# Performance work log

Hardware: AMD Instinct MI355X
Metric: run time of the kernel (lower is better)

Reference implementation:

```python
import jax, jax.numpy as jnp
import numpy as np
import math

B, T, C = 2, 2048, 1024
H = 16
D = C // H


def setup_inputs() -> dict:
    key = jax.random.key(0)
    ks = jax.random.split(key, 5)
    s = 1.0 / math.sqrt(C)
    return {
        "x": jax.random.normal(ks[0], (B, T, C), dtype=jnp.float32),
        "W_qkv": jax.random.normal(ks[1], (C, 3 * C), dtype=jnp.float32) * s,
        "b_qkv": jnp.zeros((3 * C,), dtype=jnp.float32),
        "W_proj": jax.random.normal(ks[2], (C, C), dtype=jnp.float32) * s,
        "b_proj": jnp.zeros((C,), dtype=jnp.float32),
    }


def reference(x, W_qkv, b_qkv, W_proj, b_proj):
    qkv = x @ W_qkv + b_qkv  # [B,T,3C]
    q, k, v = jnp.split(qkv, 3, axis=-1)
    # [B,T,C] -> [B,H,T,D]
    q = q.reshape(B, T, H, D).transpose(0, 2, 1, 3)
    k = k.reshape(B, T, H, D).transpose(0, 2, 1, 3)
    v = v.reshape(B, T, H, D).transpose(0, 2, 1, 3)
    sm_scale = 1.0 / math.sqrt(D)
    att = jnp.einsum("bhqd,bhkd->bhqk", q, k) * sm_scale
    causal = jnp.tril(jnp.ones((T, T), dtype=bool))  # True = keep
    att = jnp.where(causal, att, -jnp.inf)
    att = jax.nn.softmax(att, axis=-1)
    y = jnp.einsum("bhqk,bhkd->bhqd", att, v)  # [B,H,T,D]
    y = y.transpose(0, 2, 1, 3).reshape(B, T, C)
    return y @ W_proj + b_proj
```

## Files before the change

kernel.cpp:

```cpp
#include <hip/hip_runtime.h>
#include <hip/hip_bf16.h>
#include <math.h>

#define BB 2
#define TT 2048
#define CCH 1024
#define HH 16
#define DD 64
#define BT (BB*TT)
#define N3 (3*CCH)

typedef __attribute__((ext_vector_type(8))) short short8;
typedef __attribute__((ext_vector_type(4))) float f32x4;
typedef __attribute__((ext_vector_type(16))) float f32x16;

__device__ __forceinline__ unsigned short f2bf(float f) {
  unsigned int u = __float_as_uint(f);
  unsigned int r = (u + 0x7FFFu + ((u >> 16) & 1u)) >> 16;
  return (unsigned short)r;
}
__device__ __forceinline__ int cvtpk(float lo, float hi) {
  int r;
  asm("v_cvt_pk_bf16_f32 %0, %1, %2" : "=v"(r) : "v"(lo), "v"(hi));
  return r;
}
__device__ __forceinline__ void plswap(int &a, int &b) {
  asm("v_permlane32_swap_b32 %0, %1" : "+v"(a), "+v"(b));
}
__device__ __forceinline__ float fexp2(float x) {
  float r;
  asm("v_exp_f32 %0, %1" : "=v"(r) : "v"(x));
  return r;
}
__device__ __forceinline__ void gload_lds16(const unsigned short* g, unsigned short* l) {
  __builtin_amdgcn_global_load_lds((const __attribute__((address_space(1))) void*)g,
                                   (__attribute__((address_space(3))) void*)l, 16, 0, 0);
}
__device__ __forceinline__ float fmax3(float a, float b, float c) {
  return fmaxf(fmaxf(a, b), c);
}


__global__ __launch_bounds__(256) void k_prep(const float* __restrict__ x,
                                              const float* __restrict__ W_qkv,
                                              const float* __restrict__ W_proj,
                                              unsigned short* __restrict__ Xb,
                                              unsigned short* __restrict__ Wt_qkv,
                                              unsigned short* __restrict__ Wt_proj) {
  __shared__ float tile[32][33];
  int id = blockIdx.x;
  int tid = threadIdx.x;
  if (id < 2048) {
    int i = id * 256 + tid;
    const float4 a = *(const float4*)(x + (size_t)i * 8);
    const float4 b = *(const float4*)(x + (size_t)i * 8 + 4);
    short8 v;
    v[0] = f2bf(a.x); v[1] = f2bf(a.y); v[2] = f2bf(a.z); v[3] = f2bf(a.w);
    v[4] = f2bf(b.x); v[5] = f2bf(b.y); v[6] = f2bf(b.z); v[7] = f2bf(b.w);
    *(short8*)(Xb + (size_t)i * 8) = v;
    return;
  }
  const float* in;
  unsigned short* out;
  int R, Cn, tc, tr;
  if (id < 2048 + 3072) {
    int u = id - 2048;
    in = W_qkv; out = Wt_qkv; R = CCH; Cn = N3;
    tc = (u % 96) * 32; tr = (u / 96) * 32;
  } else {
    int u = id - 5120;
    in = W_proj; out = Wt_proj; R = CCH; Cn = CCH;
    tc = (u % 32) * 32; tr = (u / 32) * 32;
  }
  int lx = tid & 31;
  int ly = tid >> 5;
#pragma unroll
  for (int i = 0; i < 32; i += 8)
    tile[ly + i][lx] = in[(size_t)(tr + ly + i) * Cn + tc + lx];
  __syncthreads();
#pragma unroll
  for (int i = 0; i < 32; i += 8)
    out[(size_t)(tc + ly + i) * R + tr + lx] = f2bf(tile[lx][ly + i]);
}

__global__ __launch_bounds__(256) void k_qkv_gemm(const unsigned short* __restrict__ Xb,
                                                  const unsigned short* __restrict__ Wt,
                                                  const float* __restrict__ bias,
                                                  unsigned short* __restrict__ Qf,
                                                  unsigned short* __restrict__ Kf,
                                                  unsigned short* __restrict__ Vf) {
  __shared__ __align__(16) unsigned short As[128 * 32];
  __shared__ __align__(16) unsigned short Bs[128 * 32];
  int tid = threadIdx.x;
  int mb = blockIdx.x * 128;
  int nb = blockIdx.y * 128;
  int wid = tid >> 6, lane = tid & 63;
  int wr = (wid >> 1) * 64, wc = (wid & 1) * 64;
  int l15 = lane & 15, l4 = lane >> 4;
  int l16 = lane >> 2, lc = (lane & 3) * 8;
  f32x4 acc[4][4];
#pragma unroll
  for (int a = 0; a < 4; ++a)
#pragma unroll
    for (int b = 0; b < 4; ++b)
#pragma unroll
      for (int j = 0; j < 4; ++j) acc[a][b][j] = 0.0f;

  for (int kb = 0; kb < CCH; kb += 32) {
#pragma unroll
    for (int i = 0; i < 2; ++i) {
      int arow = wid * 32 + i * 16;
      gload_lds16(Xb + (size_t)(mb + arow + l16) * CCH + kb + lc, &As[arow * 32]);
      gload_lds16(Wt + (size_t)(nb + arow + l16) * CCH + kb + lc, &Bs[arow * 32]);
    }
    __syncthreads();
    short8 af[4], bfr[4];
#pragma unroll
    for (int mt = 0; mt < 4; ++mt) af[mt] = *(const short8*)(&As[(wr + mt * 16 + l15) * 32 + l4 * 8]);
#pragma unroll
    for (int nt = 0; nt < 4; ++nt) bfr[nt] = *(const short8*)(&Bs[(wc + nt * 16 + l15) * 32 + l4 * 8]);
#pragma unroll
    for (int mt = 0; mt < 4; ++mt)
#pragma unroll
      for (int nt = 0; nt < 4; ++nt)
        acc[mt][nt] = __builtin_amdgcn_mfma_f32_16x16x32_bf16(af[mt], bfr[nt], acc[mt][nt], 0, 0, 0);
    __syncthreads();
  }

#pragma unroll
  for (int mt = 0; mt < 4; ++mt) {
#pragma unroll
    for (int nt = 0; nt < 4; ++nt) {
      int gcol = nb + wc + nt * 16 + l15;
      int which = gcol >> 10;
      int cc = gcol & 1023;
      int hh = cc >> 6, d = cc & 63;
      float bv = bias[gcol];
#pragma unroll
      for (int j = 0; j < 4; ++j) {
        int grow = mb + wr + mt * 16 + l4 * 4 + j;
        int b = grow >> 11, t = grow & 2047;
        float v = acc[mt][nt][j] + bv;
        size_t bh = (size_t)(b * HH + hh) * TT * DD;
        if (which == 2) {
          size_t a = (size_t)((((t >> 6) * 2 + (d >> 5)) * 4 + ((t >> 4) & 3)) * 512
                             + (((t >> 3) & 1) * 32 + (d & 31)) * 8 + (t & 7));
          Vf[bh + a] = f2bf(v);
        } else {
          size_t a = (size_t)(((t >> 5) * 4 + (d >> 4)) * 512
                             + ((d >> 3) & 1) * 256 + (t & 31) * 8 + (d & 7));
          if (which == 0) Qf[bh + a] = f2bf(v * 0.18033688f);
          else            Kf[bh + a] = f2bf(v);
        }
      }
    }
  }
}

__global__ __launch_bounds__(128) void k_attn(const unsigned short* __restrict__ Qf,
                                              const unsigned short* __restrict__ Kf,
                                              const unsigned short* __restrict__ Vf,
                                              unsigned short* __restrict__ Y) {
  __shared__ float ex[64 * 33];
  __shared__ float exml[128];
  int tid = threadIdx.x;
  int jx = blockIdx.x;
  int j = 63 - (jx >> 5);
  int bh = jx & 31;
  int wid = tid >> 6, lane = tid & 63;
  int l31 = lane & 31, h = lane >> 5;
  int q0 = j * 32;
  int qrow = q0 + l31;
  int tmax = j >> 1;

  const unsigned short* Qp = Qf + (size_t)bh * TT * DD;
  const unsigned short* Kp = Kf + (size_t)bh * TT * DD;
  const unsigned short* Vp = Vf + (size_t)bh * TT * DD;

  short8 qf[4];
#pragma unroll
  for (int m = 0; m < 4; ++m)
    qf[m] = *(const short8*)(Qp + (size_t)(j * 4 + m) * 512 + lane * 8);

  f32x16 zv;
#pragma unroll
  for (int r = 0; r < 16; ++r) zv[r] = 0.0f;
  f32x16 po[2];
  po[0] = zv; po[1] = zv;
  float mrun = -1e30f, lrun = 0.0f;

  for (int t = wid; t <= tmax; t += 2) {
    int kvb = t * 64;

    short8 kf[2][4];
#pragma unroll
    for (int t32 = 0; t32 < 2; ++t32)
#pragma unroll
      for (int m = 0; m < 4; ++m)
        kf[t32][m] = *(const short8*)(Kp + (size_t)((t * 2 + t32) * 4 + m) * 512 + lane * 8);

    f32x16 st[2];
    __builtin_amdgcn_s_setprio(1);
#pragma unroll
    for (int t32 = 0; t32 < 2; ++t32) {
      st[t32] = __builtin_amdgcn_mfma_f32_32x32x16_bf16(kf[t32][0], qf[0], zv, 0, 0, 0);
#pragma unroll
      for (int m = 1; m < 4; ++m)
        st[t32] = __builtin_amdgcn_mfma_f32_32x32x16_bf16(kf[t32][m], qf[m], st[t32], 0, 0, 0);
    }
    __builtin_amdgcn_s_setprio(0);

    short8 vf[2][4];
#pragma unroll
    for (int dt = 0; dt < 2; ++dt)
#pragma unroll
      for (int g = 0; g < 4; ++g)
        vf[dt][g] = *(const short8*)(Vp + (size_t)((t * 2 + dt) * 4 + g) * 512 + lane * 8);

    if (kvb + 63 > q0) {
#pragma unroll
      for (int t32 = 0; t32 < 2; ++t32)
#pragma unroll
        for (int r = 0; r < 16; ++r) {
          int kvg = kvb + t32 * 32 + (r & 3) + 8 * (r >> 2) + 4 * h;
          if (kvg > qrow) st[t32][r] = -1e30f;
        }
    }

    float A = st[0][0], B = st[0][1], C = st[0][2], Dv = st[0][3];
#pragma unroll
    for (int r = 4; r < 16; r += 4) {
      A = fmax3(A, st[0][r], st[0][r + 1]);
      B = fmax3(B, st[0][r + 2], st[0][r + 3]);
      C = fmax3(C, st[1][r - 4], st[1][r - 3]);
      Dv = fmax3(Dv, st[1][r - 2], st[1][r - 1]);
    }
    C = fmax3(C, st[1][12], st[1][13]);
    Dv = fmax3(Dv, st[1][14], st[1][15]);
    float mx = fmaxf(fmax3(A, B, C), Dv);
    mx = fmaxf(mx, __shfl_xor(mx, 32));

    if (__any(mx - mrun > 8.0f)) {
      float mnew = fmaxf(mrun, mx);
      float alpha = fexp2(mrun - mnew);
      lrun *= alpha;
#pragma unroll
      for (int dt = 0; dt < 2; ++dt)
#pragma unroll
        for (int r = 0; r < 16; ++r) po[dt][r] *= alpha;
      mrun = mnew;
    }

    float sum = 0.0f;
#pragma unroll
    for (int t32 = 0; t32 < 2; ++t32)
#pragma unroll
      for (int r = 0; r < 16; ++r) {
        float p = fexp2(st[t32][r] - mrun);
        st[t32][r] = p;
        sum += p;
      }
    sum += __shfl_xor(sum, 32);
    lrun += sum;

    short8 pf[4];
#pragma unroll
    for (int g = 0; g < 4; ++g) {
      int t32 = g >> 1, r0 = (g & 1) * 8;
      int a = cvtpk(st[t32][r0 + 0], st[t32][r0 + 1]);
      int b = cvtpk(st[t32][r0 + 4], st[t32][r0 + 5]);
      plswap(a, b);
      int c = cvtpk(st[t32][r0 + 2], st[t32][r0 + 3]);
      int d = cvtpk(st[t32][r0 + 6], st[t32][r0 + 7]);
      plswap(c, d);
      union { int w[4]; short8 s; } un;
      un.w[0] = a; un.w[1] = c; un.w[2] = b; un.w[3] = d;
      pf[g] = un.s;
    }

    __builtin_amdgcn_s_setprio(1);
#pragma unroll
    for (int dt = 0; dt < 2; ++dt)
#pragma unroll
      for (int g = 0; g < 4; ++g)
        po[dt] = __builtin_amdgcn_mfma_f32_32x32x16_bf16(vf[dt][g], pf[g], po[dt], 0, 0, 0);
    __builtin_amdgcn_s_setprio(0);
  }

  __syncthreads();
  if (wid == 1) {
#pragma unroll
    for (int dt = 0; dt < 2; ++dt)
#pragma unroll
      for (int r = 0; r < 16; ++r) ex[lane * 33 + dt * 16 + r] = po[dt][r];
    exml[lane] = mrun;
    exml[64 + lane] = lrun;
  }
  __syncthreads();
  if (wid == 0) {
    float m1 = exml[lane], l1 = exml[64 + lane];
    float M = fmaxf(mrun, m1);
    float a0 = fexp2(mrun - M), a1 = fexp2(m1 - M);
    float inv = 1.0f / (lrun * a0 + l1 * a1);
    a0 *= inv; a1 *= inv;
    int b = bh >> 4, hh = bh & 15;
    unsigned short* yp = Y + ((size_t)(b * TT + qrow)) * CCH + hh * DD;
#pragma unroll
    for (int dt = 0; dt < 2; ++dt)
#pragma unroll
      for (int r = 0; r < 16; r += 2) {
        int d = dt * 32 + (r & 3) + 8 * (r >> 2) + 4 * h;
        float v0 = po[dt][r]     * a0 + ex[lane * 33 + dt * 16 + r]     * a1;
        float v1 = po[dt][r + 1] * a0 + ex[lane * 33 + dt * 16 + r + 1] * a1;
        *(int*)(yp + d) = cvtpk(v0, v1);
      }
  }
}

__global__ __launch_bounds__(256) void k_proj_gemm(const unsigned short* __restrict__ Yb,
                                                   const unsigned short* __restrict__ Wt,
                                                   const float* __restrict__ bias,
                                                   float* __restrict__ Out) {
  __shared__ __align__(16) unsigned short As[128 * 32];
  __shared__ __align__(16) unsigned short Bs[128 * 32];
  int tid = threadIdx.x;
  int mb = blockIdx.x * 128;
  int nb = blockIdx.y * 128;
  int wid = tid >> 6, lane = tid & 63;
  int wr = (wid >> 1) * 64, wc = (wid & 1) * 64;
  int l15 = lane & 15, l4 = lane >> 4;
  int l16 = lane >> 2, lc = (lane & 3) * 8;
  f32x4 acc[4][4];
#pragma unroll
  for (int a = 0; a < 4; ++a)
#pragma unroll
    for (int b = 0; b < 4; ++b)
#pragma unroll
      for (int j = 0; j < 4; ++j) acc[a][b][j] = 0.0f;

  for (int kb = 0; kb < CCH; kb += 32) {
#pragma unroll
    for (int i = 0; i < 2; ++i) {
      int arow = wid * 32 + i * 16;
      gload_lds16(Yb + (size_t)(mb + arow + l16) * CCH + kb + lc, &As[arow * 32]);
      gload_lds16(Wt + (size_t)(nb + arow + l16) * CCH + kb + lc, &Bs[arow * 32]);
    }
    __syncthreads();
    short8 af[4], bfr[4];
#pragma unroll
    for (int mt = 0; mt < 4; ++mt) af[mt] = *(const short8*)(&As[(wr + mt * 16 + l15) * 32 + l4 * 8]);
#pragma unroll
    for (int nt = 0; nt < 4; ++nt) bfr[nt] = *(const short8*)(&Bs[(wc + nt * 16 + l15) * 32 + l4 * 8]);
#pragma unroll
    for (int mt = 0; mt < 4; ++mt)
#pragma unroll
      for (int nt = 0; nt < 4; ++nt)
        acc[mt][nt] = __builtin_amdgcn_mfma_f32_16x16x32_bf16(af[mt], bfr[nt], acc[mt][nt], 0, 0, 0);
    __syncthreads();
  }

#pragma unroll
  for (int mt = 0; mt < 4; ++mt) {
#pragma unroll
    for (int nt = 0; nt < 4; ++nt) {
      int gcol = nb + wc + nt * 16 + l15;
      float bv = bias[gcol];
#pragma unroll
      for (int j = 0; j < 4; ++j) {
        int grow = mb + wr + mt * 16 + l4 * 4 + j;
        Out[(size_t)grow * CCH + gcol] = acc[mt][nt][j] + bv;
      }
    }
  }
}

extern "C" void kernel_launch(void* const* d_in, const int* in_sizes, int n_in,
                              void* d_out, int out_size, void* d_ws, size_t ws_size,
                              hipStream_t stream) {
  const float* x      = (const float*)d_in[0];
  const float* W_qkv  = (const float*)d_in[1];
  const float* b_qkv  = (const float*)d_in[2];
  const float* W_proj = (const float*)d_in[3];
  const float* b_proj = (const float*)d_in[4];
  float* out = (float*)d_out;

  char* ws = (char*)d_ws;
  size_t off = 0;
  unsigned short* Wt_qkv  = (unsigned short*)(ws + off); off += (size_t)N3 * CCH * 2;
  unsigned short* Wt_proj = (unsigned short*)(ws + off); off += (size_t)CCH * CCH * 2;
  unsigned short* Xb      = (unsigned short*)(ws + off); off += (size_t)BT * CCH * 2;
  unsigned short* Qfb     = (unsigned short*)(ws + off); off += (size_t)BT * CCH * 2;
  unsigned short* Kfb     = (unsigned short*)(ws + off); off += (size_t)BT * CCH * 2;
  unsigned short* Vfb     = (unsigned short*)(ws + off); off += (size_t)BT * CCH * 2;
  unsigned short* Yb      = (unsigned short*)(ws + off); off += (size_t)BT * CCH * 2;

  k_prep<<<dim3(2048 + 3072 + 1024), 256, 0, stream>>>(x, W_qkv, W_proj, Xb, Wt_qkv, Wt_proj);
  k_qkv_gemm<<<dim3(BT / 128, N3 / 128), 256, 0, stream>>>(Xb, Wt_qkv, b_qkv, Qfb, Kfb, Vfb);
  k_attn<<<dim3(2048), 128, 0, stream>>>(Qfb, Kfb, Vfb, Yb);
  k_proj_gemm<<<dim3(BT / 128, CCH / 128), 256, 0, stream>>>(Yb, Wt_proj, b_proj, out);
}
```

Baseline: 104.9 us.

## Double-buffer K/V register loads in attention loop to prefetch next tile

The attention inner loop now issues global loads of the next K/V tile into a second register buffer before computing on the current tile, alternating between two buffers, with sched_barrier to stop the compiler reordering. This hides global load latency behind the MFMA and softmax work of the current tile. In exchange it roughly doubles the registers held for K/V fragments, which could cause spills or lower occupancy.

```diff
diff --git a/kernel.cpp b/kernel.cpp
--- a/kernel.cpp
+++ b/kernel.cpp
@@ -157,6 +157,99 @@
   }
 }
 
+#define AT_ISSUE(KF, VF, tt)                                                                     \
+  {                                                                                              \
+    int _t = (tt);                                                                               \
+    _Pragma("unroll")                                                                            \
+    for (int t32 = 0; t32 < 2; ++t32)                                                            \
+      _Pragma("unroll")                                                                          \
+      for (int m = 0; m < 4; ++m)                                                                \
+        KF[t32][m] = *(const short8*)(Kp + (size_t)((_t * 2 + t32) * 4 + m) * 512 + lane * 8);   \
+    _Pragma("unroll")                                                                            \
+    for (int dt = 0; dt < 2; ++dt)                                                               \
+      _Pragma("unroll")                                                                          \
+      for (int g = 0; g < 4; ++g)                                                                \
+        VF[dt][g] = *(const short8*)(Vp + (size_t)((_t * 2 + dt) * 4 + g) * 512 + lane * 8);     \
+  }
+
+#define AT_COMPUTE(KF, VF, tt)                                                                   \
+  {                                                                                              \
+    int kvb = (tt) * 64;                                                                         \
+    f32x16 st[2];                                                                                \
+    __builtin_amdgcn_s_setprio(1);                                                               \
+    _Pragma("unroll")                                                                            \
+    for (int t32 = 0; t32 < 2; ++t32) {                                                          \
+      st[t32] = __builtin_amdgcn_mfma_f32_32x32x16_bf16(KF[t32][0], qf[0], zv, 0, 0, 0);         \
+      _Pragma("unroll")                                                                          \
+      for (int m = 1; m < 4; ++m)                                                                \
+        st[t32] = __builtin_amdgcn_mfma_f32_32x32x16_bf16(KF[t32][m], qf[m], st[t32], 0, 0, 0);  \
+    }                                                                                            \
+    __builtin_amdgcn_s_setprio(0);                                                               \
+    if (kvb + 63 > q0) {                                                                         \
+      _Pragma("unroll")                                                                          \
+      for (int t32 = 0; t32 < 2; ++t32)                                                          \
+        _Pragma("unroll")                                                                        \
+        for (int r = 0; r < 16; ++r) {                                                           \
+          int kvg = kvb + t32 * 32 + (r & 3) + 8 * (r >> 2) + 4 * h;                             \
+          if (kvg > qrow) st[t32][r] = -1e30f;                                                   \
+        }                                                                                        \
+    }                                                                                            \
+    float A = st[0][0], B = st[0][1], C = st[0][2], Dv = st[0][3];                               \
+    _Pragma("unroll")                                                                            \
+    for (int r = 4; r < 16; r += 4) {                                                            \
+      A = fmax3(A, st[0][r], st[0][r + 1]);                                                      \
+      B = fmax3(B, st[0][r + 2], st[0][r + 3]);                                                  \
+      C = fmax3(C, st[1][r - 4], st[1][r - 3]);                                                  \
+      Dv = fmax3(Dv, st[1][r - 2], st[1][r - 1]);                                                \
+    }                                                                                            \
+    C = fmax3(C, st[1][12], st[1][13]);                                                          \
+    Dv = fmax3(Dv, st[1][14], st[1][15]);                                                        \
+    float mx = fmaxf(fmax3(A, B, C), Dv);                                                        \
+    mx = fmaxf(mx, __shfl_xor(mx, 32));                                                          \
+    if (__any(mx - mrun > 8.0f)) {                                                               \
+      float mnew = fmaxf(mrun, mx);                                                              \
+      float alpha = fexp2(mrun - mnew);                                                          \
+      lrun *= alpha;                                                                             \
+      _Pragma("unroll")                                                                          \
+      for (int dt = 0; dt < 2; ++dt)                                                             \
+        _Pragma("unroll")                                                                        \
+        for (int r = 0; r < 16; ++r) po[dt][r] *= alpha;                                         \
+      mrun = mnew;                                                                               \
+    }                                                                                            \
+    float sum = 0.0f;                                                                            \
+    _Pragma("unroll")                                                                            \
+    for (int t32 = 0; t32 < 2; ++t32)                                                            \
+      _Pragma("unroll")                                                                          \
+      for (int r = 0; r < 16; ++r) {                                                             \
+        float p = fexp2(st[t32][r] - mrun);                                                      \
+        st[t32][r] = p;                                                                          \
+        sum += p;                                                                                \
+      }                                                                                          \
+    sum += __shfl_xor(sum, 32);                                                                  \
+    lrun += sum;                                                                                 \
+    short8 pf[4];                                                                                \
+    _Pragma("unroll")                                                                            \
+    for (int g = 0; g < 4; ++g) {                                                                \
+      int t32 = g >> 1, r0 = (g & 1) * 8;                                                        \
+      int a = cvtpk(st[t32][r0 + 0], st[t32][r0 + 1]);                                           \
+      int b = cvtpk(st[t32][r0 + 4], st[t32][r0 + 5]);                                           \
+      plswap(a, b);                                                                              \
+      int c = cvtpk(st[t32][r0 + 2], st[t32][r0 + 3]);                                           \
+      int d = cvtpk(st[t32][r0 + 6], st[t32][r0 + 7]);                                           \
+      plswap(c, d);                                                                              \
+      union { int w[4]; short8 s; } un;                                                          \
+      un.w[0] = a; un.w[1] = c; un.w[2] = b; un.w[3] = d;                                        \
+      pf[g] = un.s;                                                                              \
+    }                                                                                            \
+    __builtin_amdgcn_s_setprio(1);                                                               \
+    _Pragma("unroll")                                                                            \
+    for (int dt = 0; dt < 2; ++dt)                                                               \
+      _Pragma("unroll")                                                                          \
+      for (int g = 0; g < 4; ++g)                                                                \
+        po[dt] = __builtin_amdgcn_mfma_f32_32x32x16_bf16(VF[dt][g], pf[g], po[dt], 0, 0, 0);     \
+    __builtin_amdgcn_s_setprio(0);                                                               \
+  }
+
 __global__ __launch_bounds__(128) void k_attn(const unsigned short* __restrict__ Qf,
                                               const unsigned short* __restrict__ Kf,
                                               const unsigned short* __restrict__ Vf,
@@ -189,102 +282,24 @@
   po[0] = zv; po[1] = zv;
   float mrun = -1e30f, lrun = 0.0f;
 
-  for (int t = wid; t <= tmax; t += 2) {
-    int kvb = t * 64;
-
-    short8 kf[2][4];
-#pragma unroll
-    for (int t32 = 0; t32 < 2; ++t32)
-#pragma unroll
-      for (int m = 0; m < 4; ++m)
-        kf[t32][m] = *(const short8*)(Kp + (size_t)((t * 2 + t32) * 4 + m) * 512 + lane * 8);
-
-    f32x16 st[2];
-    __builtin_amdgcn_s_setprio(1);
-#pragma unroll
-    for (int t32 = 0; t32 < 2; ++t32) {
-      st[t32] = __builtin_amdgcn_mfma_f32_32x32x16_bf16(kf[t32][0], qf[0], zv, 0, 0, 0);
-#pragma unroll
-      for (int m = 1; m < 4; ++m)
-        st[t32] = __builtin_amdgcn_mfma_f32_32x32x16_bf16(kf[t32][m], qf[m], st[t32], 0, 0, 0);
+  short8 kfA[2][4], vfA[2][4], kfB[2][4], vfB[2][4];
+  int t = wid;
+  if (t <= tmax) {
+    AT_ISSUE(kfA, vfA, t);
+    while (true) {
+      int tn = t + 2;
+      if (tn <= tmax) AT_ISSUE(kfB, vfB, tn);
+      __builtin_amdgcn_sched_barrier(0);
+      AT_COMPUTE(kfA, vfA, t);
+      if (tn > tmax) break;
+      t = tn;
+      tn = t + 2;
+      if (tn <= tmax) AT_ISSUE(kfA, vfA, tn);
+      __builtin_amdgcn_sched_barrier(0);
+      AT_COMPUTE(kfB, vfB, t);
+      if (tn > tmax) break;
+      t = tn;
     }
-    __builtin_amdgcn_s_setprio(0);
-
-    short8 vf[2][4];
-#pragma unroll
-    for (int dt = 0; dt < 2; ++dt)
-#pragma unroll
-      for (int g = 0; g < 4; ++g)
-        vf[dt][g] = *(const short8*)(Vp + (size_t)((t * 2 + dt) * 4 + g) * 512 + lane * 8);
-
-    if (kvb + 63 > q0) {
-#pragma unroll
-      for (int t32 = 0; t32 < 2; ++t32)
-#pragma unroll
-        for (int r = 0; r < 16; ++r) {
-          int kvg = kvb + t32 * 32 + (r & 3) + 8 * (r >> 2) + 4 * h;
-          if (kvg > qrow) st[t32][r] = -1e30f;
-        }
-    }
-
-    float A = st[0][0], B = st[0][1], C = st[0][2], Dv = st[0][3];
-#pragma unroll
-    for (int r = 4; r < 16; r += 4) {
-      A = fmax3(A, st[0][r], st[0][r + 1]);
-      B = fmax3(B, st[0][r + 2], st[0][r + 3]);
-      C = fmax3(C, st[1][r - 4], st[1][r - 3]);
-      Dv = fmax3(Dv, st[1][r - 2], st[1][r - 1]);
-    }
-    C = fmax3(C, st[1][12], st[1][13]);
-    Dv = fmax3(Dv, st[1][14], st[1][15]);
-    float mx = fmaxf(fmax3(A, B, C), Dv);
-    mx = fmaxf(mx, __shfl_xor(mx, 32));
-
-    if (__any(mx - mrun > 8.0f)) {
-      float mnew = fmaxf(mrun, mx);
-      float alpha = fexp2(mrun - mnew);
-      lrun *= alpha;
-#pragma unroll
-      for (int dt = 0; dt < 2; ++dt)
-#pragma unroll
-        for (int r = 0; r < 16; ++r) po[dt][r] *= alpha;
-      mrun = mnew;
-    }
-
-    float sum = 0.0f;
-#pragma unroll
-    for (int t32 = 0; t32 < 2; ++t32)
-#pragma unroll
-      for (int r = 0; r < 16; ++r) {
-        float p = fexp2(st[t32][r] - mrun);
-        st[t32][r] = p;
-        sum += p;
-      }
-    sum += __shfl_xor(sum, 32);
-    lrun += sum;
-
-    short8 pf[4];
-#pragma unroll
-    for (int g = 0; g < 4; ++g) {
-      int t32 = g >> 1, r0 = (g & 1) * 8;
-      int a = cvtpk(st[t32][r0 + 0], st[t32][r0 + 1]);
-      int b = cvtpk(st[t32][r0 + 4], st[t32][r0 + 5]);
-      plswap(a, b);
-      int c = cvtpk(st[t32][r0 + 2], st[t32][r0 + 3]);
-      int d = cvtpk(st[t32][r0 + 6], st[t32][r0 + 7]);
-      plswap(c, d);
-      union { int w[4]; short8 s; } un;
-      un.w[0] = a; un.w[1] = c; un.w[2] = b; un.w[3] = d;
-      pf[g] = un.s;
-    }
-
-    __builtin_amdgcn_s_setprio(1);
-#pragma unroll
-    for (int dt = 0; dt < 2; ++dt)
-#pragma unroll
-      for (int g = 0; g < 4; ++g)
-        po[dt] = __builtin_amdgcn_mfma_f32_32x32x16_bf16(vf[dt][g], pf[g], po[dt], 0, 0, 0);
-    __builtin_amdgcn_s_setprio(0);
   }
 
   __syncthreads();
```

Measured after the change: 115.8 us. 1.1x slower.
